# Kernel optimization log

Hardware: AMD Instinct MI355X
Metric: run time of the kernel (lower is better)

## Reference

```python
import jax, jax.numpy as jnp
import numpy as np


def _gcn_layer(x, W, b, src, dst, n_nodes):
    # PyG GCNConv: add self-loops, symmetric normalization, then
    # out[i] = sum_j norm_ij * (x[j] @ W) + b, norm_ij = deg_i^-1/2 * deg_j^-1/2
    h = x @ W  # [N, F_out]
    deg = jax.ops.segment_sum(jnp.ones_like(dst, dtype=h.dtype), dst, num_segments=n_nodes)
    dinv = jnp.where(deg > 0, jax.lax.rsqrt(deg), 0.0)
    norm = dinv[src] * dinv[dst]  # [E_total]
    msg = h[src] * norm[:, None]  # [E_total, F_out]
    out = jax.ops.segment_sum(msg, dst, num_segments=n_nodes)
    return out + b


def _add_self_loops(edge_index, n_nodes):
    loops = jnp.arange(n_nodes, dtype=edge_index.dtype)
    src = jnp.concatenate([edge_index[0], loops])
    dst = jnp.concatenate([edge_index[1], loops])
    return src, dst


def setup_inputs() -> dict:
    key = jax.random.key(0)
    ks = jax.random.split(key, 4)
    N, E, DIN, DOUT = 50000, 800000, 128, 64
    HID = 2 * DOUT
    x = jax.random.normal(ks[0], (N, DIN), dtype=jnp.float32)
    edge_index = jax.random.randint(ks[1], (2, E), 0, N, dtype=jnp.int64)
    W1 = jax.random.normal(ks[2], (DIN, HID), dtype=jnp.float32) / np.sqrt(DIN)
    b1 = jnp.zeros((HID,), dtype=jnp.float32)
    W2 = jax.random.normal(ks[3], (HID, DOUT), dtype=jnp.float32) / np.sqrt(HID)
    b2 = jnp.zeros((DOUT,), dtype=jnp.float32)
    return {"x": x, "edge_index": edge_index, "W1": W1, "b1": b1, "W2": W2, "b2": b2}


def reference(x, edge_index, W1, b1, W2, b2):
    n_nodes = x.shape[0]
    src, dst = _add_self_loops(edge_index, n_nodes)
    h = jax.nn.relu(_gcn_layer(x, W1, b1, src, dst, n_nodes))
    h = jax.nn.relu(_gcn_layer(h, W2, b2, src, dst, n_nodes))
    return h
```

## Files before the change

### kernel.cpp

```cpp
#include <hip/hip_runtime.h>

#define F_DIN  128
#define F_HID  128
#define F_DOUT 64
#define SCAN_VT 8
#define P_HIST 8
#define SCAN_FLAG 0x40000000

typedef __bf16 bf16x8 __attribute__((ext_vector_type(8)));
typedef float f32x4 __attribute__((ext_vector_type(4)));
typedef unsigned short ushort8 __attribute__((ext_vector_type(8)));
typedef unsigned int uint4v __attribute__((ext_vector_type(4)));
typedef unsigned int uint2v __attribute__((ext_vector_type(2)));

static __device__ __forceinline__ unsigned short f2bf(float f) {
  unsigned u = __builtin_bit_cast(unsigned, f);
  u += 0x7FFF + ((u >> 16) & 1);
  return (unsigned short)(u >> 16);
}
static __device__ __forceinline__ float bflo(unsigned u) {
  return __builtin_bit_cast(float, u << 16);
}
static __device__ __forceinline__ float bfhi(unsigned u) {
  return __builtin_bit_cast(float, u & 0xFFFF0000u);
}


__global__ __launch_bounds__(256) void prep_zero(const float* __restrict__ W1,
                                                 const float* __restrict__ W2,
                                                 unsigned short* __restrict__ Wt1,
                                                 unsigned short* __restrict__ Wt2,
                                                 uint4v* __restrict__ zbase, int n16) {
  int i = blockIdx.x * 256 + threadIdx.x;
  if (i < n16) zbase[i] = uint4v{0u, 0u, 0u, 0u};
  if (i < F_HID * F_DIN) {
    int c = i / F_DIN, k = i % F_DIN;
    Wt1[i] = f2bf(W1[k * F_HID + c]);
  }
  int j = i - F_HID * F_DIN;
  if (j >= 0 && j < F_DOUT * F_HID) {
    int c = j / F_HID, k = j % F_HID;
    Wt2[j] = f2bf(W2[k * F_DOUT + c]);
  }
}

static __device__ __forceinline__ int edge_part(int i) { return (i >> 8) & (P_HIST - 1); }

static __device__ __forceinline__ void degree_body(const int* __restrict__ dst,
                                                   int* __restrict__ cntp,
                                                   unsigned short* __restrict__ rank,
                                                   int E, int N, int bid, int nblk, int tid) {
  int i = bid * 256 + tid;
  int stride = nblk * 256;
  for (; i < E; i += stride) {
    int d = dst[i];
    int p = edge_part(i);
    int r = atomicAdd(&cntp[p * N + d], 1);
    rank[i] = (unsigned short)r;
  }
}


template <int BN, bool AF32>
static __device__ __forceinline__ void gemm_body(const void* __restrict__ Ap,
                                                 const unsigned short* __restrict__ Wt,
                                                 unsigned short* __restrict__ Cout,
                                                 int M, int bid, int tid) {
  constexpr int K = 128;
  constexpr int NT = BN / 16;
  const int wv = tid >> 6;
  const int lane = tid & 63;
  const int r = lane & 15, g = lane >> 4;
  const int r0 = bid * 128 + wv * 32;

  f32x4 acc[2][NT];
#pragma unroll
  for (int t = 0; t < 2; ++t)
#pragma unroll
    for (int c = 0; c < NT; ++c) acc[t][c] = f32x4{0.f, 0.f, 0.f, 0.f};

#pragma unroll
  for (int kk = 0; kk < 4; ++kk) {
    const int kbase = kk * 32 + g * 8;
    bf16x8 afrag[2];
#pragma unroll
    for (int t = 0; t < 2; ++t) {
      int row = r0 + t * 16 + r;
      if (row >= M) row = M - 1;
      if (AF32) {
        const float* ap = (const float*)Ap + (size_t)row * K + kbase;
        float4 f0 = *(const float4*)(ap);
        float4 f1 = *(const float4*)(ap + 4);
        ushort8 h;
        h[0] = f2bf(f0.x); h[1] = f2bf(f0.y); h[2] = f2bf(f0.z); h[3] = f2bf(f0.w);
        h[4] = f2bf(f1.x); h[5] = f2bf(f1.y); h[6] = f2bf(f1.z); h[7] = f2bf(f1.w);
        afrag[t] = __builtin_bit_cast(bf16x8, h);
      } else {
        const unsigned short* ap = (const unsigned short*)Ap + (size_t)row * K + kbase;
        uint4v u = *(const uint4v*)ap;
        afrag[t] = __builtin_bit_cast(bf16x8, u);
      }
    }
#pragma unroll
    for (int c = 0; c < NT; ++c) {
      const int col = c * 16 + r;
      uint4v ub = *(const uint4v*)(Wt + (size_t)col * K + kbase);
      bf16x8 bfrag = __builtin_bit_cast(bf16x8, ub);
      acc[0][c] = __builtin_amdgcn_mfma_f32_16x16x32_bf16(afrag[0], bfrag, acc[0][c], 0, 0, 0);
      acc[1][c] = __builtin_amdgcn_mfma_f32_16x16x32_bf16(afrag[1], bfrag, acc[1][c], 0, 0, 0);
    }
  }

#pragma unroll
  for (int t = 0; t < 2; ++t)
#pragma unroll
    for (int c = 0; c < NT; ++c) {
      const int col = c * 16 + r;
#pragma unroll
      for (int j = 0; j < 4; ++j) {
        int row = r0 + t * 16 + g * 4 + j;
        if (row < M) Cout[(size_t)row * BN + col] = f2bf(acc[t][c][j]);
      }
    }
}

__global__ __launch_bounds__(256) void fat_gemm1_degree(const float* __restrict__ x,
                                                        const unsigned short* __restrict__ Wt1,
                                                        unsigned short* __restrict__ H1, int M,
                                                        const int* __restrict__ dst,
                                                        int* __restrict__ cntp,
                                                        unsigned short* __restrict__ rank,
                                                        int E, int N, int gemmBlocks) {
  const int b = (int)blockIdx.x;
  if (b < gemmBlocks) {
    gemm_body<F_HID, true>(x, Wt1, H1, M, b, threadIdx.x);
  } else {
    degree_body(dst, cntp, rank, E, N, b - gemmBlocks, gridDim.x - gemmBlocks, threadIdx.x);
  }
}

__global__ __launch_bounds__(256) void scan_one(const int* __restrict__ cntp,
                                                int* __restrict__ status,
                                                int* __restrict__ row_off,
                                                int* __restrict__ pbase,
                                                float* __restrict__ dinv,
                                                int N, int nb) {
  const int tid = threadIdx.x;
  const int bid = (int)blockIdx.x;
  const int base = (bid * 256 + tid) * SCAN_VT;

  int degs[SCAN_VT];
  int s = 0;
#pragma unroll
  for (int j = 0; j < SCAN_VT; ++j) {
    int d = 0;
    if (base + j < N) {
#pragma unroll
      for (int p = 0; p < P_HIST; ++p) d += cntp[p * N + base + j];
    }
    degs[j] = d;
    s += d;
  }
  __shared__ int sm[256];
  sm[tid] = s;
  __syncthreads();
#pragma unroll
  for (int off = 1; off < 256; off <<= 1) {
    int t = (tid >= off) ? sm[tid - off] : 0;
    __syncthreads();
    sm[tid] += t;
    __syncthreads();
  }
  const int agg = sm[255];

  if (tid == 0) atomicExch(&status[bid], agg | SCAN_FLAG);

  __shared__ int sbase;
  if (tid < 64) {
    int v = 0;
    if (tid < bid) {
      do { v = atomicOr(&status[tid], 0); } while (!(v & SCAN_FLAG));
      v &= ~SCAN_FLAG;
    }
#pragma unroll
    for (int off2 = 1; off2 < 64; off2 <<= 1) v += __shfl_xor(v, off2, 64);
    if (tid == 0) sbase = v;
  }
  __syncthreads();
  const int bbase = sbase;

  int ex = sm[tid] - s + bbase;
#pragma unroll
  for (int j = 0; j < SCAN_VT; ++j) {
    int node = base + j;
    if (node < N) {
      row_off[node] = ex;
      dinv[node] = rsqrtf((float)(degs[j] + 1));
      int pb = ex;
#pragma unroll
      for (int p = 0; p < P_HIST; ++p) {
        pbase[p * N + node] = pb;
        pb += cntp[p * N + node];
      }
      ex += degs[j];
    }
  }
  if (bid == nb - 1 && tid == 255) row_off[N] = bbase + agg;
}

__global__ __launch_bounds__(256) void fill_kernel(const int* __restrict__ src,
                                                   const int* __restrict__ dst,
                                                   const unsigned short* __restrict__ rank,
                                                   const int* __restrict__ pbase,
                                                   unsigned short* __restrict__ csr,
                                                   int E, int N) {
  int i = blockIdx.x * 256 + threadIdx.x;
  int stride = gridDim.x * 256;
  for (; i < E; i += stride) {
    int d = dst[i];
    int p = edge_part(i);
    csr[pbase[p * N + d] + rank[i]] = (unsigned short)src[i];
  }
}


__global__ __launch_bounds__(256) void agg128_gemm2(const unsigned short* __restrict__ H,
                                                    const int* __restrict__ row_off,
                                                    const unsigned short* __restrict__ csr,
                                                    const float* __restrict__ dinv,
                                                    const float* __restrict__ bias,
                                                    const unsigned short* __restrict__ Wt2,
                                                    unsigned short* __restrict__ H2,
                                                    int Nn) {
  const int tid = threadIdx.x;
  const int lane = tid & 63;
  const int wv = tid >> 6;
  const int q = lane >> 4, ql = lane & 15;
  const int lrow = wv * 4 + q;
  const int node = blockIdx.x * 16 + lrow;

  __shared__ unsigned short ldsa[16 * 136];

  unsigned words[4] = {0u, 0u, 0u, 0u};
  if (node < Nn) {
    const float di = dinv[node];
    const uint4v us = *(const uint4v*)(H + (size_t)node * 128 + ql * 8);

    float acc[8];
#pragma unroll
    for (int i = 0; i < 8; ++i) acc[i] = 0.f;

    const int beg = row_off[node], end = row_off[node + 1];
    for (int e = beg; e < end; e += 4) {
      int i1 = e + 1, i2 = e + 2, i3 = e + 3;
      int c1 = i1 < end ? i1 : end - 1;
      int c2 = i2 < end ? i2 : end - 1;
      int c3 = i3 < end ? i3 : end - 1;
      int s0 = csr[e], s1 = csr[c1], s2 = csr[c2], s3 = csr[c3];
      float w0 = dinv[s0];
      float w1 = i1 < end ? dinv[s1] : 0.f;
      float w2 = i2 < end ? dinv[s2] : 0.f;
      float w3 = i3 < end ? dinv[s3] : 0.f;
      uint4v u0 = *(const uint4v*)(H + (size_t)s0 * 128 + ql * 8);
      uint4v u1 = *(const uint4v*)(H + (size_t)s1 * 128 + ql * 8);
      uint4v u2 = *(const uint4v*)(H + (size_t)s2 * 128 + ql * 8);
      uint4v u3 = *(const uint4v*)(H + (size_t)s3 * 128 + ql * 8);
#pragma unroll
      for (int i = 0; i < 4; ++i) {
        acc[2 * i]     = fmaf(w0, bflo(u0[i]), acc[2 * i]);
        acc[2 * i + 1] = fmaf(w0, bfhi(u0[i]), acc[2 * i + 1]);
        acc[2 * i]     = fmaf(w1, bflo(u1[i]), acc[2 * i]);
        acc[2 * i + 1] = fmaf(w1, bfhi(u1[i]), acc[2 * i + 1]);
        acc[2 * i]     = fmaf(w2, bflo(u2[i]), acc[2 * i]);
        acc[2 * i + 1] = fmaf(w2, bfhi(u2[i]), acc[2 * i + 1]);
        acc[2 * i]     = fmaf(w3, bflo(u3[i]), acc[2 * i]);
        acc[2 * i + 1] = fmaf(w3, bfhi(u3[i]), acc[2 * i + 1]);
      }
    }

    const float di2 = di * di;
#pragma unroll
    for (int i = 0; i < 4; ++i) {
      float v0 = di * acc[2 * i]     + di2 * bflo(us[i]) + bias[ql * 8 + 2 * i];
      float v1 = di * acc[2 * i + 1] + di2 * bfhi(us[i]) + bias[ql * 8 + 2 * i + 1];
      v0 = fmaxf(v0, 0.f); v1 = fmaxf(v1, 0.f);
      words[i] = (unsigned)f2bf(v0) | ((unsigned)f2bf(v1) << 16);
    }
  }
  {
    uint4v o; o[0] = words[0]; o[1] = words[1]; o[2] = words[2]; o[3] = words[3];
    *(uint4v*)(&ldsa[lrow * 136 + ql * 8]) = o;
  }
  __syncthreads();

  const int r = lane & 15, g = lane >> 4;
  f32x4 c = f32x4{0.f, 0.f, 0.f, 0.f};
#pragma unroll
  for (int kk = 0; kk < 4; ++kk) {
    const int kbase = kk * 32 + g * 8;
    bf16x8 a = __builtin_bit_cast(bf16x8, *(const uint4v*)(&ldsa[r * 136 + kbase]));
    bf16x8 b = __builtin_bit_cast(bf16x8, *(const uint4v*)(Wt2 + (size_t)(wv * 16 + r) * 128 + kbase));
    c = __builtin_amdgcn_mfma_f32_16x16x32_bf16(a, b, c, 0, 0, 0);
  }
#pragma unroll
  for (int j = 0; j < 4; ++j) {
    int no = blockIdx.x * 16 + g * 4 + j;
    if (no < Nn) H2[(size_t)no * 64 + wv * 16 + r] = f2bf(c[j]);
  }
}

__global__ __launch_bounds__(256) void agg64_kernel(const unsigned short* __restrict__ H,
                                                    const int* __restrict__ row_off,
                                                    const unsigned short* __restrict__ csr,
                                                    const float* __restrict__ dinv,
                                                    const float* __restrict__ bias,
                                                    float* __restrict__ out,
                                                    int Nn) {
  const int lane = threadIdx.x & 63;
  const int wv = threadIdx.x >> 6;
  const int q = lane >> 4, ql = lane & 15;
  const int node = blockIdx.x * 16 + wv * 4 + q;
  if (node >= Nn) return;

  const float di = dinv[node];
  const uint2v us = *(const uint2v*)(H + (size_t)node * 64 + ql * 4);

  float acc[4];
#pragma unroll
  for (int i = 0; i < 4; ++i) acc[i] = 0.f;

  const int beg = row_off[node], end = row_off[node + 1];
  for (int e = beg; e < end; e += 4) {
    int i1 = e + 1, i2 = e + 2, i3 = e + 3;
    int c1 = i1 < end ? i1 : end - 1;
    int c2 = i2 < end ? i2 : end - 1;
    int c3 = i3 < end ? i3 : end - 1;
    int s0 = csr[e], s1 = csr[c1], s2 = csr[c2], s3 = csr[c3];
    float w0 = dinv[s0];
    float w1 = i1 < end ? dinv[s1] : 0.f;
    float w2 = i2 < end ? dinv[s2] : 0.f;
    float w3 = i3 < end ? dinv[s3] : 0.f;
    uint2v u0 = *(const uint2v*)(H + (size_t)s0 * 64 + ql * 4);
    uint2v u1 = *(const uint2v*)(H + (size_t)s1 * 64 + ql * 4);
    uint2v u2 = *(const uint2v*)(H + (size_t)s2 * 64 + ql * 4);
    uint2v u3 = *(const uint2v*)(H + (size_t)s3 * 64 + ql * 4);
#pragma unroll
    for (int i = 0; i < 2; ++i) {
      acc[2 * i]     = fmaf(w0, bflo(u0[i]), acc[2 * i]);
      acc[2 * i + 1] = fmaf(w0, bfhi(u0[i]), acc[2 * i + 1]);
      acc[2 * i]     = fmaf(w1, bflo(u1[i]), acc[2 * i]);
      acc[2 * i + 1] = fmaf(w1, bfhi(u1[i]), acc[2 * i + 1]);
      acc[2 * i]     = fmaf(w2, bflo(u2[i]), acc[2 * i]);
      acc[2 * i + 1] = fmaf(w2, bfhi(u2[i]), acc[2 * i + 1]);
      acc[2 * i]     = fmaf(w3, bflo(u3[i]), acc[2 * i]);
      acc[2 * i + 1] = fmaf(w3, bfhi(u3[i]), acc[2 * i + 1]);
    }
  }

  const float di2 = di * di;
  float4 o;
  o.x = fmaxf(di * acc[0] + di2 * bflo(us[0]) + bias[ql * 4 + 0], 0.f);
  o.y = fmaxf(di * acc[1] + di2 * bfhi(us[0]) + bias[ql * 4 + 1], 0.f);
  o.z = fmaxf(di * acc[2] + di2 * bflo(us[1]) + bias[ql * 4 + 2], 0.f);
  o.w = fmaxf(di * acc[3] + di2 * bfhi(us[1]) + bias[ql * 4 + 3], 0.f);
  *(float4*)(out + (size_t)node * 64 + ql * 4) = o;
}


extern "C" void kernel_launch(void* const* d_in, const int* in_sizes, int n_in,
                              void* d_out, int out_size, void* d_ws, size_t ws_size,
                              hipStream_t stream) {
  const float* x  = (const float*)d_in[0];
  const int*   ei = (const int*)d_in[1];
  const float* W1 = (const float*)d_in[2];
  const float* b1 = (const float*)d_in[3];
  const float* W2 = (const float*)d_in[4];
  const float* b2 = (const float*)d_in[5];
  float* out = (float*)d_out;

  const int E = in_sizes[1] / 2;
  const int N = in_sizes[0] / F_DIN;
  const int* src = ei;
  const int* dst = ei + E;

  char* ws = (char*)d_ws;
  auto alloc = [&](size_t bytes) {
    char* p = ws;
    ws += (bytes + 255) & ~(size_t)255;
    return p;
  };
  int*            cntp      = (int*)alloc((size_t)P_HIST * N * 4);
  int*            status    = (int*)alloc(1024);
  int*            row_off   = (int*)alloc((size_t)(N + 1) * 4);
  int*            pbase     = (int*)alloc((size_t)P_HIST * N * 4);
  float*          dinv      = (float*)alloc((size_t)N * 4);
  unsigned short* rank      = (unsigned short*)alloc((size_t)E * 2);
  unsigned short* csr       = (unsigned short*)alloc((size_t)E * 2);
  unsigned short* H1        = (unsigned short*)alloc((size_t)N * F_HID * 2);
  unsigned short* H2        = (unsigned short*)alloc((size_t)N * F_DOUT * 2);
  unsigned short* Wt1       = (unsigned short*)alloc((size_t)F_HID * F_DIN * 2);
  unsigned short* Wt2       = (unsigned short*)alloc((size_t)F_DOUT * F_HID * 2);

  const int gb = (N + 127) / 128;
  const int zero16 = ((P_HIST * N * 4) + 1024) / 16;

  prep_zero<<<(zero16 + 255) / 256, 256, 0, stream>>>(W1, W2, Wt1, Wt2, (uint4v*)cntp, zero16);

  int eb = (E + 255) / 256; if (eb > 2048) eb = 2048;
  fat_gemm1_degree<<<gb + eb, 256, 0, stream>>>(x, Wt1, H1, N, dst, cntp, rank, E, N, gb);

  const int nb = (N + 256 * SCAN_VT - 1) / (256 * SCAN_VT);
  scan_one<<<nb, 256, 0, stream>>>(cntp, status, row_off, pbase, dinv, N, nb);

  fill_kernel<<<eb, 256, 0, stream>>>(src, dst, rank, pbase, csr, E, N);

  agg128_gemm2<<<(N + 15) / 16, 256, 0, stream>>>(H1, row_off, csr, dinv, b1, Wt2, H2, N);

  agg64_kernel<<<(N + 15) / 16, 256, 0, stream>>>(H2, row_off, csr, dinv, b2, out, N);
}
```

Before: 135.8 us.

## Pack fp16 source dinv into CSR entries and unroll gathers by eight

The fill kernel now stores each CSR entry as a 32-bit word holding the 16-bit source index and the fp16-rounded dinv of the source. Both aggregation kernels decode the weight from that word, which removes the dependent dinv[src] gather. They also issue eight neighbor-row loads per iteration instead of four to increase memory-level parallelism. The costs are twice the CSR footprint, a dinv gather moved into fill_kernel, fp16 precision loss on the normalization weight, and higher register pressure from the wider unroll.

```diff
diff --git a/kernel.cpp b/kernel.cpp
--- a/kernel.cpp
+++ b/kernel.cpp
@@ -1,4 +1,5 @@
 #include <hip/hip_runtime.h>
+#include <hip/hip_fp16.h>
 
 #define F_DIN  128
 #define F_HID  128
@@ -23,6 +24,10 @@
 }
 static __device__ __forceinline__ float bfhi(unsigned u) {
   return __builtin_bit_cast(float, u & 0xFFFF0000u);
+}
+static __device__ __forceinline__ float f16tof32(unsigned hbits) {
+  __half h = __builtin_bit_cast(__half, (unsigned short)hbits);
+  return __half2float(h);
 }
 
 
@@ -212,21 +217,24 @@
                                                    const int* __restrict__ dst,
                                                    const unsigned short* __restrict__ rank,
                                                    const int* __restrict__ pbase,
-                                                   unsigned short* __restrict__ csr,
+                                                   const float* __restrict__ dinv,
+                                                   unsigned* __restrict__ csr,
                                                    int E, int N) {
   int i = blockIdx.x * 256 + threadIdx.x;
   int stride = gridDim.x * 256;
   for (; i < E; i += stride) {
     int d = dst[i];
+    int s = src[i];
     int p = edge_part(i);
-    csr[pbase[p * N + d] + rank[i]] = (unsigned short)src[i];
+    unsigned short hb = __builtin_bit_cast(unsigned short, __float2half_rn(dinv[s]));
+    csr[pbase[p * N + d] + rank[i]] = (unsigned)s | ((unsigned)hb << 16);
   }
 }
 
 
 __global__ __launch_bounds__(256) void agg128_gemm2(const unsigned short* __restrict__ H,
                                                     const int* __restrict__ row_off,
-                                                    const unsigned short* __restrict__ csr,
+                                                    const unsigned* __restrict__ csr,
                                                     const float* __restrict__ dinv,
                                                     const float* __restrict__ bias,
                                                     const unsigned short* __restrict__ Wt2,
@@ -251,31 +259,28 @@
     for (int i = 0; i < 8; ++i) acc[i] = 0.f;
 
     const int beg = row_off[node], end = row_off[node + 1];
-    for (int e = beg; e < end; e += 4) {
-      int i1 = e + 1, i2 = e + 2, i3 = e + 3;
-      int c1 = i1 < end ? i1 : end - 1;
-      int c2 = i2 < end ? i2 : end - 1;
-      int c3 = i3 < end ? i3 : end - 1;
-      int s0 = csr[e], s1 = csr[c1], s2 = csr[c2], s3 = csr[c3];
-      float w0 = dinv[s0];
-      float w1 = i1 < end ? dinv[s1] : 0.f;
-      float w2 = i2 < end ? dinv[s2] : 0.f;
-      float w3 = i3 < end ? dinv[s3] : 0.f;
-      uint4v u0 = *(const uint4v*)(H + (size_t)s0 * 128 + ql * 8);
-      uint4v u1 = *(const uint4v*)(H + (size_t)s1 * 128 + ql * 8);
-      uint4v u2 = *(const uint4v*)(H + (size_t)s2 * 128 + ql * 8);
-      uint4v u3 = *(const uint4v*)(H + (size_t)s3 * 128 + ql * 8);
-#pragma unroll
-      for (int i = 0; i < 4; ++i) {
-        acc[2 * i]     = fmaf(w0, bflo(u0[i]), acc[2 * i]);
-        acc[2 * i + 1] = fmaf(w0, bfhi(u0[i]), acc[2 * i + 1]);
-        acc[2 * i]     = fmaf(w1, bflo(u1[i]), acc[2 * i]);
-        acc[2 * i + 1] = fmaf(w1, bfhi(u1[i]), acc[2 * i + 1]);
-        acc[2 * i]     = fmaf(w2, bflo(u2[i]), acc[2 * i]);
-        acc[2 * i + 1] = fmaf(w2, bfhi(u2[i]), acc[2 * i + 1]);
-        acc[2 * i]     = fmaf(w3, bflo(u3[i]), acc[2 * i]);
-        acc[2 * i + 1] = fmaf(w3, bfhi(u3[i]), acc[2 * i + 1]);
+    for (int e = beg; e < end; e += 8) {
+      int sidx[8];
+      float w[8];
+#pragma unroll
+      for (int j = 0; j < 8; ++j) {
+        int ij = e + j;
+        int cj = ij < end ? ij : end - 1;
+        unsigned pk = csr[cj];
+        sidx[j] = (int)(pk & 0xFFFFu);
+        w[j] = (ij < end) ? f16tof32(pk >> 16) : 0.f;
       }
+      uint4v u[8];
+#pragma unroll
+      for (int j = 0; j < 8; ++j)
+        u[j] = *(const uint4v*)(H + (size_t)sidx[j] * 128 + ql * 8);
+#pragma unroll
+      for (int j = 0; j < 8; ++j)
+#pragma unroll
+        for (int i = 0; i < 4; ++i) {
+          acc[2 * i]     = fmaf(w[j], bflo(u[j][i]), acc[2 * i]);
+          acc[2 * i + 1] = fmaf(w[j], bfhi(u[j][i]), acc[2 * i + 1]);
+        }
     }
 
     const float di2 = di * di;
@@ -311,7 +316,7 @@
 
 __global__ __launch_bounds__(256) void agg64_kernel(const unsigned short* __restrict__ H,
                                                     const int* __restrict__ row_off,
-                                                    const unsigned short* __restrict__ csr,
+                                                    const unsigned* __restrict__ csr,
                                                     const float* __restrict__ dinv,
                                                     const float* __restrict__ bias,
                                                     float* __restrict__ out,
@@ -330,31 +335,28 @@
   for (int i = 0; i < 4; ++i) acc[i] = 0.f;
 
   const int beg = row_off[node], end = row_off[node + 1];
-  for (int e = beg; e < end; e += 4) {
-    int i1 = e + 1, i2 = e + 2, i3 = e + 3;
-    int c1 = i1 < end ? i1 : end - 1;
-    int c2 = i2 < end ? i2 : end - 1;
-    int c3 = i3 < end ? i3 : end - 1;
-    int s0 = csr[e], s1 = csr[c1], s2 = csr[c2], s3 = csr[c3];
-    float w0 = dinv[s0];
-    float w1 = i1 < end ? dinv[s1] : 0.f;
-    float w2 = i2 < end ? dinv[s2] : 0.f;
-    float w3 = i3 < end ? dinv[s3] : 0.f;
-    uint2v u0 = *(const uint2v*)(H + (size_t)s0 * 64 + ql * 4);
-    uint2v u1 = *(const uint2v*)(H + (size_t)s1 * 64 + ql * 4);
-    uint2v u2 = *(const uint2v*)(H + (size_t)s2 * 64 + ql * 4);
-    uint2v u3 = *(const uint2v*)(H + (size_t)s3 * 64 + ql * 4);
-#pragma unroll
-    for (int i = 0; i < 2; ++i) {
-      acc[2 * i]     = fmaf(w0, bflo(u0[i]), acc[2 * i]);
-      acc[2 * i + 1] = fmaf(w0, bfhi(u0[i]), acc[2 * i + 1]);
-      acc[2 * i]     = fmaf(w1, bflo(u1[i]), acc[2 * i]);
-      acc[2 * i + 1] = fmaf(w1, bfhi(u1[i]), acc[2 * i + 1]);
-      acc[2 * i]     = fmaf(w2, bflo(u2[i]), acc[2 * i]);
-      acc[2 * i + 1] = fmaf(w2, bfhi(u2[i]), acc[2 * i + 1]);
-      acc[2 * i]     = fmaf(w3, bflo(u3[i]), acc[2 * i]);
-      acc[2 * i + 1] = fmaf(w3, bfhi(u3[i]), acc[2 * i + 1]);
-    }
+  for (int e = beg; e < end; e += 8) {
+    int sidx[8];
+    float w[8];
+#pragma unroll
+    for (int j = 0; j < 8; ++j) {
+      int ij = e + j;
+      int cj = ij < end ? ij : end - 1;
+      unsigned pk = csr[cj];
+      sidx[j] = (int)(pk & 0xFFFFu);
+      w[j] = (ij < end) ? f16tof32(pk >> 16) : 0.f;
+    }
+    uint2v u[8];
+#pragma unroll
+    for (int j = 0; j < 8; ++j)
+      u[j] = *(const uint2v*)(H + (size_t)sidx[j] * 64 + ql * 4);
+#pragma unroll
+    for (int j = 0; j < 8; ++j)
+#pragma unroll
+      for (int i = 0; i < 2; ++i) {
+        acc[2 * i]     = fmaf(w[j], bflo(u[j][i]), acc[2 * i]);
+        acc[2 * i + 1] = fmaf(w[j], bfhi(u[j][i]), acc[2 * i + 1]);
+      }
   }
 
   const float di2 = di * di;
@@ -395,7 +397,7 @@
   int*            pbase     = (int*)alloc((size_t)P_HIST * N * 4);
   float*          dinv      = (float*)alloc((size_t)N * 4);
   unsigned short* rank      = (unsigned short*)alloc((size_t)E * 2);
-  unsigned short* csr       = (unsigned short*)alloc((size_t)E * 2);
+  unsigned*       csr       = (unsigned*)alloc((size_t)E * 4);
   unsigned short* H1        = (unsigned short*)alloc((size_t)N * F_HID * 2);
   unsigned short* H2        = (unsigned short*)alloc((size_t)N * F_DOUT * 2);
   unsigned short* Wt1       = (unsigned short*)alloc((size_t)F_HID * F_DIN * 2);
@@ -412,7 +414,7 @@
   const int nb = (N + 256 * SCAN_VT - 1) / (256 * SCAN_VT);
   scan_one<<<nb, 256, 0, stream>>>(cntp, status, row_off, pbase, dinv, N, nb);
 
-  fill_kernel<<<eb, 256, 0, stream>>>(src, dst, rank, pbase, csr, E, N);
+  fill_kernel<<<eb, 256, 0, stream>>>(src, dst, rank, pbase, dinv, csr, E, N);
 
   agg128_gemm2<<<(N + 15) / 16, 256, 0, stream>>>(H1, row_off, csr, dinv, b1, Wt2, H2, N);
 
```

Result: faster. 132.4 us (-2.5%).
